# Performance work log

Measured on AMD Instinct MI355X. Metric: run time of the kernel, lower is better.

## Reference

```python
import jax, jax.numpy as jnp
import numpy as np

B_, J_, D_, E_, N_, K_ = 32, 1024, 192, 384, 16, 3


def _dwconv(x, w, b):
    # x: (B,J,E), w: (E,1,K) depthwise, b: (E,)
    xc = jnp.transpose(x, (0, 2, 1))  # (B,E,J)
    pad = w.shape[2] // 2
    y = jax.lax.conv_general_dilated(
        xc, w, window_strides=(1,), padding=[(pad, pad)],
        feature_group_count=w.shape[0], dimension_numbers=('NCH', 'OIH', 'NCH'))
    return jnp.transpose(y + b[None, :, None], (0, 2, 1))  # (B,J,E)


def _scan_dir(x, cw, cb, WB, bB, WC, bC, WD, bD, A, Wi, bi, Wr, br):
    # One directional selective-SSM pass. x: (B,J,E); A: (N,) negative diag.
    xc = _dwconv(x, cw, cb)                       # (B,J,E)
    Bt = xc @ WB + bB                             # (B,J,N)
    Ct = xc @ WC + bC                             # (B,J,N)
    Dt = jax.nn.softplus(xc @ WD + bD)            # Delta, (B,J,N)
    A_bar = jnp.exp(Dt * A)                       # ZOH discretization
    B_bar = (A_bar - 1.0) / (A + 1e-6) * Bt
    u = xc @ Wi + bi                              # in_to_state, (B,J,N)
    Bu = B_bar * u

    def step(h, ab_bu):
        ab, bu = ab_bu
        h = ab * h + bu
        return h, h

    h0 = jnp.zeros((x.shape[0], A.shape[0]), x.dtype)
    _, hs = jax.lax.scan(step, h0, (jnp.swapaxes(A_bar, 0, 1), jnp.swapaxes(Bu, 0, 1)))
    hs = jnp.swapaxes(hs, 0, 1)                   # (B,J,N)
    return (hs * Ct) @ Wr + br                    # readout, (B,J,E)


def setup_inputs() -> dict:
    key = jax.random.key(0)
    ks = iter(jax.random.split(key, 40))

    def nrm(shape, scale=0.02):
        return jax.random.normal(next(ks), shape, jnp.float32) * scale

    inp = {
        'tokens': jax.random.normal(next(ks), (B_, J_, D_), jnp.float32),
        'norm_g': jnp.ones((D_,), jnp.float32),
        'norm_b': jnp.zeros((D_,), jnp.float32),
        'Wx': nrm((D_, E_)), 'bx': jnp.zeros((E_,), jnp.float32),
        'Wz': nrm((D_, E_)), 'bz': jnp.zeros((E_,), jnp.float32),
        'convf_w': nrm((E_, 1, K_), 0.1), 'convf_b': jnp.zeros((E_,), jnp.float32),
        'convb_w': nrm((E_, 1, K_), 0.1), 'convb_b': jnp.zeros((E_,), jnp.float32),
        'WBf': nrm((E_, N_)), 'bBf': jnp.zeros((N_,), jnp.float32),
        'WCf': nrm((E_, N_)), 'bCf': jnp.zeros((N_,), jnp.float32),
        'WDf': nrm((E_, N_)), 'bDf': jnp.zeros((N_,), jnp.float32),
        'WBb': nrm((E_, N_)), 'bBb': jnp.zeros((N_,), jnp.float32),
        'WCb': nrm((E_, N_)), 'bCb': jnp.zeros((N_,), jnp.float32),
        'WDb': nrm((E_, N_)), 'bDb': jnp.zeros((N_,), jnp.float32),
        'A_log': nrm((N_,), 0.5),
        'Wi': nrm((E_, N_)), 'bi': jnp.zeros((N_,), jnp.float32),
        'Wr': nrm((N_, E_)), 'br': jnp.zeros((E_,), jnp.float32),
        'Wo': nrm((E_, D_)), 'bo': jnp.zeros((D_,), jnp.float32),
    }
    return inp


def reference(tokens, norm_g, norm_b, Wx, bx, Wz, bz, convf_w, convf_b,
              convb_w, convb_b, WBf, bBf, WCf, bCf, WDf, bDf, WBb, bBb,
              WCb, bCb, WDb, bDb, A_log, Wi, bi, Wr, br, Wo, bo):
    # LayerNorm (biased variance, eps=1e-5, like torch)
    mu = jnp.mean(tokens, axis=-1, keepdims=True)
    var = jnp.mean(jnp.square(tokens - mu), axis=-1, keepdims=True)
    t = (tokens - mu) / jnp.sqrt(var + 1e-5) * norm_g + norm_b

    x = t @ Wx + bx
    z = t @ Wz + bz
    gate = jax.nn.sigmoid(jax.nn.silu(z))

    # A computed under no_grad in torch -> stop_gradient here
    A = jax.lax.stop_gradient(-jax.nn.softplus(A_log))

    y_f = _scan_dir(x, convf_w, convf_b, WBf, bBf, WCf, bCf, WDf, bDf, A, Wi, bi, Wr, br)
    y_b = jnp.flip(_scan_dir(jnp.flip(x, 1), convb_w, convb_b, WBb, bBb, WCb, bCb,
                             WDb, bDb, A, Wi, bi, Wr, br), 1)
    y = (y_f + y_b) * gate
    return tokens + y @ Wo + bo
```

## Files before the change

kernel.cpp:

```cpp
#include <hip/hip_runtime.h>
#include <math.h>


typedef __attribute__((ext_vector_type(8))) short short8;
typedef __attribute__((ext_vector_type(4))) float f32x4;

__device__ __forceinline__ unsigned short f2bf(float f){
  union { float f; unsigned u; } v; v.f = f;
  unsigned r = v.u + 0x7FFFu + ((v.u >> 16) & 1u);
  return (unsigned short)(r >> 16);
}
__device__ __forceinline__ float bf2f(unsigned short s){
  union { unsigned u; float f; } v; v.u = ((unsigned)s) << 16;
  return v.f;
}
__device__ __forceinline__ float softplusf(float x){
  return (x > 20.f) ? x : log1pf(expf(x));
}
__device__ __forceinline__ float sigf_fast(float x){
  return __builtin_amdgcn_rcpf(1.f + __expf(-x));
}

__global__ __launch_bounds__(256) void prep_kernel(
    const float* __restrict__ Wx, const float* __restrict__ Wz,
    const float* __restrict__ WBf, const float* __restrict__ WCf,
    const float* __restrict__ WDf, const float* __restrict__ WBb,
    const float* __restrict__ WCb, const float* __restrict__ WDb,
    const float* __restrict__ Wi, const float* __restrict__ Wr,
    const float* __restrict__ Wo,
    const float* __restrict__ bBf, const float* __restrict__ bCf,
    const float* __restrict__ bDf, const float* __restrict__ bBb,
    const float* __restrict__ bCb, const float* __restrict__ bDb,
    const float* __restrict__ bi,
    unsigned short* __restrict__ Wxz_t, unsigned short* __restrict__ W4f_t,
    unsigned short* __restrict__ W4b_t, unsigned short* __restrict__ Wrt2,
    unsigned short* __restrict__ Wot, float* __restrict__ b4f,
    float* __restrict__ b4b)
{
  int idx = blockIdx.x * 256 + threadIdx.x;
  if (idx < 147456){ int n = idx / 192, k = idx % 192;
    Wxz_t[idx] = f2bf(n < 384 ? Wx[k*384 + n] : Wz[k*384 + n - 384]); return; }
  idx -= 147456;
  if (idx < 24576){ int n = idx / 384, k = idx % 384;
    const float* W = (n<16)?WBf:(n<32)?WCf:(n<48)?WDf:Wi;
    W4f_t[idx] = f2bf(W[k*16 + (n&15)]); return; }
  idx -= 24576;
  if (idx < 24576){ int n = idx / 384, k = idx % 384;
    const float* W = (n<16)?WBb:(n<32)?WCb:(n<48)?WDb:Wi;
    W4b_t[idx] = f2bf(W[k*16 + (n&15)]); return; }
  idx -= 24576;
  if (idx < 12288){ int n = idx / 32, k = idx % 32;
    Wrt2[idx] = f2bf(Wr[(k&15)*384 + n]); return; }
  idx -= 12288;
  if (idx < 73728){ int n = idx / 384, k = idx % 384;
    Wot[idx] = f2bf(Wo[k*192 + n]); return; }
  idx -= 73728;
  if (idx < 64){
    const float* bsel = (idx<16)?bBf:(idx<32)?bCf:(idx<48)?bDf:bi;
    b4f[idx] = bsel[idx & 15]; return; }
  idx -= 64;
  if (idx < 64){
    const float* bsel = (idx<16)?bBb:(idx<32)?bCb:(idx<48)?bDb:bi;
    b4b[idx] = bsel[idx & 15]; return; }
}

__global__ __launch_bounds__(256, 2) void ln_xz_mfma(
    const float* __restrict__ tokens, const float* __restrict__ g,
    const float* __restrict__ nb, const unsigned short* __restrict__ Wxz_t,
    const float* __restrict__ bx, const float* __restrict__ bz,
    unsigned short* __restrict__ x_bf, unsigned short* __restrict__ gate_bf)
{
  __shared__ unsigned short t_lds[64 * 200];
  const int t = threadIdx.x;
  const int ch = blockIdx.x & 1;
  const int row0 = (blockIdx.x >> 1) * 64;

  {
#pragma unroll
    for (int p = 0; p < 2; p++){
      const int r = p*32 + (t >> 3), l8 = t & 7;
      const float* tr = tokens + (long)(row0 + r) * 192;
      float v[24], s = 0.f, sq = 0.f;
#pragma unroll
      for (int i = 0; i < 24; i++){ float x = tr[l8 + 8*i]; v[i] = x; s += x; sq += x*x; }
#pragma unroll
      for (int m = 1; m < 8; m <<= 1){ s += __shfl_xor(s, m); sq += __shfl_xor(sq, m); }
      const float mu = s * (1.f/192.f);
      const float rstd = rsqrtf(sq * (1.f/192.f) - mu*mu + 1e-5f);
#pragma unroll
      for (int i = 0; i < 24; i++){
        const int d = l8 + 8*i;
        t_lds[r*200 + d] = f2bf((v[i] - mu)*rstd*g[d] + nb[d]);
      }
    }
  }
  __syncthreads();

  const int lane = t & 63, w = t >> 6;
  const int c0 = w * 96;
  const int l15 = lane & 15, q = lane >> 4;
  f32x4 acc[4][6];
#pragma unroll
  for (int m = 0; m < 4; m++)
#pragma unroll
    for (int n = 0; n < 6; n++) acc[m][n] = (f32x4){0.f,0.f,0.f,0.f};

  const unsigned short* wb = Wxz_t + (long)(ch*384 + c0 + l15)*192 + q*8;
#pragma unroll
  for (int ks = 0; ks < 6; ks++){
    const int k0 = ks * 32;
    short8 a0 = *(const short8*)&t_lds[(     l15)*200 + k0 + q*8];
    short8 a1 = *(const short8*)&t_lds[(16 + l15)*200 + k0 + q*8];
    short8 a2 = *(const short8*)&t_lds[(32 + l15)*200 + k0 + q*8];
    short8 a3 = *(const short8*)&t_lds[(48 + l15)*200 + k0 + q*8];
#pragma unroll
    for (int nf = 0; nf < 6; nf++){
      short8 bw = *(const short8*)&wb[nf*16*192 + k0];
      acc[0][nf] = __builtin_amdgcn_mfma_f32_16x16x32_bf16(a0, bw, acc[0][nf], 0, 0, 0);
      acc[1][nf] = __builtin_amdgcn_mfma_f32_16x16x32_bf16(a1, bw, acc[1][nf], 0, 0, 0);
      acc[2][nf] = __builtin_amdgcn_mfma_f32_16x16x32_bf16(a2, bw, acc[2][nf], 0, 0, 0);
      acc[3][nf] = __builtin_amdgcn_mfma_f32_16x16x32_bf16(a3, bw, acc[3][nf], 0, 0, 0);
    }
  }
  __syncthreads();

  const float* bias = ch ? bz : bx;
  unsigned short* outp = ch ? gate_bf : x_bf;
  unsigned short* stage = t_lds;

#pragma unroll
  for (int pp = 0; pp < 2; pp++){
#pragma unroll
    for (int mm = 0; mm < 2; mm++){
      const int m = pp*2 + mm;
#pragma unroll
      for (int nf = 0; nf < 6; nf++){
        const int lc = c0 + nf*16 + l15;
        const int scol = c0 + ((nf + q) % 6)*16 + l15;
        const float bv = bias[lc];
        if (ch == 0){
#pragma unroll
          for (int r = 0; r < 4; r++)
            stage[(mm*16 + q*4 + r)*392 + scol] = f2bf(acc[m][nf][r] + bv);
        } else {
#pragma unroll
          for (int r = 0; r < 4; r++){
            const float z = acc[m][nf][r] + bv;
            const float si = z * sigf_fast(z);
            stage[(mm*16 + q*4 + r)*392 + scol] = f2bf(sigf_fast(si));
          }
        }
      }
    }
    __syncthreads();
    {
#pragma unroll
      for (int i = 0; i < 6; i++){
        const int item = i*256 + t;
        const int row  = item / 48;
        const int c_out = (item % 48) * 8;
        const int qq = (row >> 2) & 3;
        const int wsl = c_out / 96;
        const int nfl = (c_out % 96) / 16;
        const int scol = wsl*96 + ((nfl + qq) % 6)*16 + (c_out % 16);
        short8 v = *(const short8*)&stage[row*392 + scol];
        const long R = (long)row0 + pp*32 + row;
        *(short8*)&outp[R*384 + c_out] = v;
      }
    }
    __syncthreads();
  }
}

__global__ __launch_bounds__(256) void proj_mfma(
    const unsigned short* __restrict__ x_bf,
    const float* __restrict__ cwf, const float* __restrict__ cbf,
    const float* __restrict__ cwb, const float* __restrict__ cbb,
    const unsigned short* __restrict__ W4f, const unsigned short* __restrict__ W4b,
    const float* __restrict__ b4f, const float* __restrict__ b4b,
    const float* __restrict__ A_log,
    float* __restrict__ Af, float* __restrict__ Buf, float* __restrict__ Ctf,
    float* __restrict__ Ab, float* __restrict__ Bub, float* __restrict__ Ctb)
{
  __shared__ unsigned short xc[64 * 392];
  float* trans = (float*)xc;
  const int t = threadIdx.x;
  const int dir = blockIdx.x >> 9;
  const int bid = blockIdx.x & 511;
  const int b  = bid >> 4;
  const int j0 = (bid & 15) * 64;
  const float* cw = dir ? cwb : cwf;
  const float* cb = dir ? cbb : cbf;
  const unsigned short* W4 = dir ? W4b : W4f;
  const float* b4 = dir ? b4b : b4f;
  float* Aout = dir ? Ab  : Af;
  float* Bout = dir ? Bub : Buf;
  float* Cout = dir ? Ctb : Ctf;

  {
    const long xrow = (long)b * 1024 * 384;
#pragma unroll
    for (int i = 0; i < 12; i++){
      const int idx = i*256 + t;
      const int r = idx / 48;
      const int e0 = (idx - r*48) * 8;
      const int jp = j0 + r;
      short8 xm = (short8){0,0,0,0,0,0,0,0};
      short8 xp = (short8){0,0,0,0,0,0,0,0};
      if (jp >= 1){
        const int js = dir ? 1024 - jp : jp - 1;
        xm = *(const short8*)&x_bf[xrow + (long)js*384 + e0];
      }
      short8 x0;
      {
        const int js = dir ? 1023 - jp : jp;
        x0 = *(const short8*)&x_bf[xrow + (long)js*384 + e0];
      }
      if (jp <= 1022){
        const int js = dir ? 1022 - jp : jp + 1;
        xp = *(const short8*)&x_bf[xrow + (long)js*384 + e0];
      }
      float wv[24], cbv[8];
#pragma unroll
      for (int v = 0; v < 6; v++)
        *(float4*)&wv[v*4] = *(const float4*)&cw[e0*3 + v*4];
#pragma unroll
      for (int v = 0; v < 2; v++)
        *(float4*)&cbv[v*4] = *(const float4*)&cb[e0 + v*4];
      short8 o;
#pragma unroll
      for (int m = 0; m < 8; m++){
        const float acc = fmaf(wv[3*m],   bf2f((unsigned short)xm[m]),
                          fmaf(wv[3*m+1], bf2f((unsigned short)x0[m]),
                          fmaf(wv[3*m+2], bf2f((unsigned short)xp[m]), cbv[m])));
        o[m] = (short)f2bf(acc);
      }
      *(short8*)&xc[r*392 + e0] = o;
    }
  }
  __syncthreads();

  const int lane = t & 63, w = t >> 6;
  const int l15 = lane & 15, q = lane >> 4;
  f32x4 acc[4];
#pragma unroll
  for (int nf = 0; nf < 4; nf++) acc[nf] = (f32x4){0.f,0.f,0.f,0.f};
  const unsigned short* wb = W4 + (long)l15*384 + q*8;
#pragma unroll
  for (int ks = 0; ks < 12; ks++){
    const int k0 = ks * 32;
    short8 a = *(const short8*)&xc[(w*16 + l15)*392 + k0 + q*8];
#pragma unroll
    for (int nf = 0; nf < 4; nf++){
      short8 bw = *(const short8*)&wb[nf*16*384 + k0];
      acc[nf] = __builtin_amdgcn_mfma_f32_16x16x32_bf16(a, bw, acc[nf], 0, 0, 0);
    }
  }
  __syncthreads();

  {
    const int n = l15;
    const float Av = -softplusf(A_log[n]);
    const float bB = b4[n], bC = b4[16+n], bD = b4[32+n], bU = b4[48+n];
#pragma unroll
    for (int r = 0; r < 4; r++){
      const int row = w*16 + q*4 + r;
      const float Bt  = acc[0][r] + bB;
      const float Ctv = acc[1][r] + bC;
      const float dt  = softplusf(acc[2][r] + bD);
      const float u   = acc[3][r] + bU;
      const float ab  = expf(dt * Av);
      const float bu  = (ab - 1.f) / (Av + 1e-6f) * Bt * u;
      trans[(0*16 + n)*66 + row] = ab;
      trans[(1*16 + n)*66 + row] = bu;
      trans[(2*16 + n)*66 + row] = Ctv;
    }
  }
  __syncthreads();

  {
    const int j = t & 63, n4 = t >> 6;
#pragma unroll
    for (int i = 0; i < 4; i++){
      const int n = n4*4 + i;
      const int jp = j0 + j;
      const long base = ((long)b*16 + n) * 1024;
      Aout[base + jp] = trans[(0*16 + n)*66 + j];
      Bout[base + jp] = trans[(1*16 + n)*66 + j];
      Cout[base + (dir ? 1023 - jp : jp)] = trans[(2*16 + n)*66 + j];
    }
  }
}

__global__ __launch_bounds__(256) void scan2_kernel(
    const float* __restrict__ Af, const float* __restrict__ Buf, float* __restrict__ hsf,
    const float* __restrict__ Ab, const float* __restrict__ Bub, float* __restrict__ hsb)
{
  __shared__ float sA[256], sB[256];
  const int sel = blockIdx.x >> 9;
  const long base = (long)(blockIdx.x & 511) * 1024;
  const float* Abar = sel ? Ab  : Af;
  const float* Bu   = sel ? Bub : Buf;
  float* hs         = sel ? hsb : hsf;
  const int t = threadIdx.x;
  const float4 a4 = *reinterpret_cast<const float4*>(&Abar[base + t*4]);
  const float4 b4 = *reinterpret_cast<const float4*>(&Bu[base + t*4]);
  float A = a4.x, Bc = b4.x;
  Bc = fmaf(a4.y, Bc, b4.y); A *= a4.y;
  Bc = fmaf(a4.z, Bc, b4.z); A *= a4.z;
  Bc = fmaf(a4.w, Bc, b4.w); A *= a4.w;
  sA[t] = A; sB[t] = Bc;
  __syncthreads();
  for (int off = 1; off < 256; off <<= 1){
    const float cA = sA[t], cB = sB[t];
    float pA = 1.f, pB = 0.f;
    if (t >= off){ pA = sA[t - off]; pB = sB[t - off]; }
    __syncthreads();
    sA[t] = pA * cA;
    sB[t] = fmaf(cA, pB, cB);
    __syncthreads();
  }
  float h = (t > 0) ? sB[t - 1] : 0.f;
  float4 o;
  h = fmaf(a4.x, h, b4.x); o.x = h;
  h = fmaf(a4.y, h, b4.y); o.y = h;
  h = fmaf(a4.z, h, b4.z); o.z = h;
  h = fmaf(a4.w, h, b4.w); o.w = h;
  *reinterpret_cast<float4*>(&hs[base + t*4]) = o;
}

__global__ __launch_bounds__(256) void final_mfma(
    const float* __restrict__ tokens, const unsigned short* __restrict__ gate_bf,
    const float* __restrict__ hsf, const float* __restrict__ Ctf,
    const float* __restrict__ hsb, const float* __restrict__ Ctb,
    const unsigned short* __restrict__ Wrt2, const float* __restrict__ br,
    const unsigned short* __restrict__ Wot, const float* __restrict__ bo,
    float* __restrict__ out)
{
  __shared__ unsigned short s2[32 * 40];
  __shared__ unsigned short yg[32 * 392];
  const int t = threadIdx.x;
  const int b  = blockIdx.x >> 5;
  const int j0 = (blockIdx.x & 31) * 32;

  {
#pragma unroll
    for (int i = 0; i < 4; i++){
      const int idx = i*256 + t;
      const int j = idx & 31, kk = idx >> 5;
      float val;
      if (kk < 16){
        const long p = ((long)b*16 + kk)*1024 + j0 + j;
        val = hsf[p] * Ctf[p];
      } else {
        const long basen = ((long)b*16 + (kk - 16)) * 1024;
        val = hsb[basen + 1023 - (j0 + j)] * Ctb[basen + j0 + j];
      }
      s2[j*40 + kk] = f2bf(val);
    }
  }
  __syncthreads();

  const int lane = t & 63, w = t >> 6;
  const int l15 = lane & 15, q = lane >> 4;
  const int rt = w & 1;
  const int ng = w >> 1;

  {
    short8 a = *(const short8*)&s2[(rt*16 + l15)*40 + q*8];
    const unsigned short* wbp = Wrt2 + (long)l15*32 + q*8;
#pragma unroll
    for (int i = 0; i < 12; i++){
      const int nf = ng*12 + i;
      short8 bw = *(const short8*)&wbp[nf*16*32];
      f32x4 acc = (f32x4){0.f,0.f,0.f,0.f};
      acc = __builtin_amdgcn_mfma_f32_16x16x32_bf16(a, bw, acc, 0, 0, 0);
      const int c = nf*16 + l15;
      const float brv = 2.f * br[c];
#pragma unroll
      for (int r = 0; r < 4; r++)
        yg[(rt*16 + q*4 + r)*392 + c] = f2bf(acc[r] + brv);
    }
  }
  __syncthreads();

  {
#pragma unroll
    for (int i = 0; i < 6; i++){
      const int item = i*256 + t;
      const int row = item / 48;
      const int cb  = (item % 48) * 8;
      short8 y8 = *(const short8*)&yg[row*392 + cb];
      short8 g8 = *(const short8*)&gate_bf[((long)b*1024 + j0 + row)*384 + cb];
      short8 o;
#pragma unroll
      for (int m = 0; m < 8; m++)
        o[m] = (short)f2bf(bf2f((unsigned short)y8[m]) * bf2f((unsigned short)g8[m]));
      *(short8*)&yg[row*392 + cb] = o;
    }
  }
  __syncthreads();

  f32x4 acc[6];
  {
#pragma unroll
    for (int i = 0; i < 6; i++) acc[i] = (f32x4){0.f,0.f,0.f,0.f};
    const unsigned short* wbp = Wot + (long)l15*384 + q*8;
#pragma unroll
    for (int ks = 0; ks < 12; ks++){
      const int k0 = ks * 32;
      short8 a = *(const short8*)&yg[(rt*16 + l15)*392 + k0 + q*8];
#pragma unroll
      for (int i = 0; i < 6; i++){
        const int nf = ng*6 + i;
        short8 bw = *(const short8*)&wbp[(long)nf*16*384 + k0];
        acc[i] = __builtin_amdgcn_mfma_f32_16x16x32_bf16(a, bw, acc[i], 0, 0, 0);
      }
    }
  }
  __syncthreads();

  float* stg = (float*)yg;
  {
    const int gq = q ^ (q >> 1);
#pragma unroll
    for (int i = 0; i < 6; i++){
      const int nf = ng*6 + i;
      const int c = nf*16 + l15;
      const float bv = bo[c];
      const int scol = ((nf + gq) % 12)*16 + l15;
#pragma unroll
      for (int r = 0; r < 4; r++)
        stg[(rt*16 + q*4 + r)*196 + scol] = acc[i][r] + bv;
    }
  }
  __syncthreads();

  {
#pragma unroll
    for (int i = 0; i < 6; i++){
      const int item = i*256 + t;
      const int row = item / 48;
      const int c4  = (item % 48) * 4;
      const int qq = (row >> 2) & 3;
      const int gg = qq ^ (qq >> 1);
      const int nf = c4 / 16;
      const int scol = ((nf + gg) % 12)*16 + (c4 % 16);
      float4 v = *(const float4*)&stg[row*196 + scol];
      const long R = (long)b*1024 + j0 + row;
      const float4 tk = *(const float4*)&tokens[R*192 + c4];
      v.x += tk.x; v.y += tk.y; v.z += tk.z; v.w += tk.w;
      *(float4*)&out[R*192 + c4] = v;
    }
  }
}

extern "C" void kernel_launch(void* const* d_in, const int* in_sizes, int n_in,
                              void* d_out, int out_size, void* d_ws, size_t ws_size,
                              hipStream_t stream)
{
  const float* tokens  = (const float*)d_in[0];
  const float* norm_g  = (const float*)d_in[1];
  const float* norm_b  = (const float*)d_in[2];
  const float* Wx      = (const float*)d_in[3];
  const float* bx      = (const float*)d_in[4];
  const float* Wz      = (const float*)d_in[5];
  const float* bz      = (const float*)d_in[6];
  const float* convf_w = (const float*)d_in[7];
  const float* convf_b = (const float*)d_in[8];
  const float* convb_w = (const float*)d_in[9];
  const float* convb_b = (const float*)d_in[10];
  const float* WBf     = (const float*)d_in[11];
  const float* bBf     = (const float*)d_in[12];
  const float* WCf     = (const float*)d_in[13];
  const float* bCf     = (const float*)d_in[14];
  const float* WDf     = (const float*)d_in[15];
  const float* bDf     = (const float*)d_in[16];
  const float* WBb     = (const float*)d_in[17];
  const float* bBb     = (const float*)d_in[18];
  const float* WCb     = (const float*)d_in[19];
  const float* bCb     = (const float*)d_in[20];
  const float* WDb     = (const float*)d_in[21];
  const float* bDb     = (const float*)d_in[22];
  const float* A_log   = (const float*)d_in[23];
  const float* Wi      = (const float*)d_in[24];
  const float* bi      = (const float*)d_in[25];
  const float* Wr      = (const float*)d_in[26];
  const float* br      = (const float*)d_in[27];
  const float* Wo      = (const float*)d_in[28];
  const float* bo      = (const float*)d_in[29];

  char* ws = (char*)d_ws;
  unsigned short* x_bf    = (unsigned short*)(ws + 0);
  unsigned short* gate_bf = (unsigned short*)(ws + 25165824);
  unsigned short* Wxz_t   = (unsigned short*)(ws + 50331648);
  unsigned short* W4f_t   = (unsigned short*)(ws + 50626560);
  unsigned short* W4b_t   = (unsigned short*)(ws + 50675712);
  unsigned short* Wrt2    = (unsigned short*)(ws + 50724864);
  unsigned short* Wot     = (unsigned short*)(ws + 50749440);
  float* b4f = (float*)(ws + 50896896);
  float* b4b = (float*)(ws + 50897152);
  float* Af  = (float*)(ws + 50897408);
  float* Buf = (float*)(ws + 52994560);
  float* Ctf = (float*)(ws + 55091712);
  float* hsf = (float*)(ws + 57188864);
  float* Ab  = (float*)(ws + 59286016);
  float* Bub = (float*)(ws + 61383168);
  float* Ctb = (float*)(ws + 63480320);
  float* hsb = (float*)(ws + 65577472);

  prep_kernel<<<1105, 256, 0, stream>>>(Wx, Wz, WBf, WCf, WDf, WBb, WCb, WDb,
                                        Wi, Wr, Wo, bBf, bCf, bDf, bBb, bCb, bDb, bi,
                                        Wxz_t, W4f_t, W4b_t, Wrt2, Wot, b4f, b4b);
  ln_xz_mfma<<<1024, 256, 0, stream>>>(tokens, norm_g, norm_b, Wxz_t, bx, bz,
                                       x_bf, gate_bf);
  proj_mfma<<<1024, 256, 0, stream>>>(x_bf, convf_w, convf_b, convb_w, convb_b,
                                      W4f_t, W4b_t, b4f, b4b, A_log,
                                      Af, Buf, Ctf, Ab, Bub, Ctb);
  scan2_kernel<<<1024, 256, 0, stream>>>(Af, Buf, hsf, Ab, Bub, hsb);
  final_mfma<<<1024, 256, 0, stream>>>(tokens, gate_bf, hsf, Ctf, hsb, Ctb,
                                       Wrt2, br, Wot, bo, (float*)d_out);
}
```

Measured before the change: 147.1 us.

## Split LayerNorm from x/z GEMM and retile GEMM to 64x128 column tiles

```diff
diff --git a/kernel.cpp b/kernel.cpp
--- a/kernel.cpp
+++ b/kernel.cpp
@@ -64,57 +64,84 @@
     b4b[idx] = bsel[idx & 15]; return; }
 }
 
-__global__ __launch_bounds__(256, 2) void ln_xz_mfma(
+__global__ __launch_bounds__(256) void ln_kernel(
     const float* __restrict__ tokens, const float* __restrict__ g,
-    const float* __restrict__ nb, const unsigned short* __restrict__ Wxz_t,
+    const float* __restrict__ nb, unsigned short* __restrict__ t_bf)
+{
+  __shared__ unsigned short s[32 * 200];
+  const int t = threadIdx.x;
+  const int row0 = blockIdx.x * 32;
+  {
+    const int r = t >> 3, l8 = t & 7;
+    const float* tr = tokens + (long)(row0 + r) * 192;
+    float v[24], sm = 0.f, sq = 0.f;
+#pragma unroll
+    for (int i = 0; i < 24; i++){ float x = tr[l8 + 8*i]; v[i] = x; sm += x; sq += x*x; }
+#pragma unroll
+    for (int m = 1; m < 8; m <<= 1){ sm += __shfl_xor(sm, m); sq += __shfl_xor(sq, m); }
+    const float mu = sm * (1.f/192.f);
+    const float rstd = rsqrtf(sq * (1.f/192.f) - mu*mu + 1e-5f);
+#pragma unroll
+    for (int i = 0; i < 24; i++){
+      const int d = l8 + 8*i;
+      s[r*200 + d] = f2bf((v[i] - mu)*rstd*g[d] + nb[d]);
+    }
+  }
+  __syncthreads();
+  {
+#pragma unroll
+    for (int i = 0; i < 3; i++){
+      const int item = i*256 + t;
+      const int row = item / 24, c8 = item % 24;
+      *(short8*)&t_bf[(long)(row0 + row)*192 + c8*8] =
+          *(const short8*)&s[row*200 + c8*8];
+    }
+  }
+}
+
+__global__ __launch_bounds__(256) void xz_gemm(
+    const unsigned short* __restrict__ t_bf,
+    const unsigned short* __restrict__ Wxz_t,
     const float* __restrict__ bx, const float* __restrict__ bz,
     unsigned short* __restrict__ x_bf, unsigned short* __restrict__ gate_bf)
 {
-  __shared__ unsigned short t_lds[64 * 200];
+  __shared__ unsigned short tl[64 * 200];
   const int t = threadIdx.x;
-  const int ch = blockIdx.x & 1;
-  const int row0 = (blockIdx.x >> 1) * 64;
-
-  {
-#pragma unroll
-    for (int p = 0; p < 2; p++){
-      const int r = p*32 + (t >> 3), l8 = t & 7;
-      const float* tr = tokens + (long)(row0 + r) * 192;
-      float v[24], s = 0.f, sq = 0.f;
-#pragma unroll
-      for (int i = 0; i < 24; i++){ float x = tr[l8 + 8*i]; v[i] = x; s += x; sq += x*x; }
-#pragma unroll
-      for (int m = 1; m < 8; m <<= 1){ s += __shfl_xor(s, m); sq += __shfl_xor(sq, m); }
-      const float mu = s * (1.f/192.f);
-      const float rstd = rsqrtf(sq * (1.f/192.f) - mu*mu + 1e-5f);
-#pragma unroll
-      for (int i = 0; i < 24; i++){
-        const int d = l8 + 8*i;
-        t_lds[r*200 + d] = f2bf((v[i] - mu)*rstd*g[d] + nb[d]);
-      }
+  const int ct = blockIdx.x % 6;
+  const int rt = blockIdx.x / 6;
+  const int row0 = rt * 64;
+
+  {
+#pragma unroll
+    for (int i = 0; i < 6; i++){
+      const int item = i*256 + t;
+      const int row = item / 24, c8 = item % 24;
+      *(short8*)&tl[row*200 + c8*8] =
+          *(const short8*)&t_bf[(long)(row0 + row)*192 + c8*8];
     }
   }
   __syncthreads();
 
   const int lane = t & 63, w = t >> 6;
-  const int c0 = w * 96;
   const int l15 = lane & 15, q = lane >> 4;
-  f32x4 acc[4][6];
+  const int C0 = ct*128 + w*32;
+
+  f32x4 acc[4][2];
 #pragma unroll
   for (int m = 0; m < 4; m++)
 #pragma unroll
-    for (int n = 0; n < 6; n++) acc[m][n] = (f32x4){0.f,0.f,0.f,0.f};
-
-  const unsigned short* wb = Wxz_t + (long)(ch*384 + c0 + l15)*192 + q*8;
+    for (int nf = 0; nf < 2; nf++) acc[m][nf] = (f32x4){0.f,0.f,0.f,0.f};
+
+  const unsigned short* wb = Wxz_t + (long)(C0 + l15)*192 + q*8;
 #pragma unroll
   for (int ks = 0; ks < 6; ks++){
     const int k0 = ks * 32;
-    short8 a0 = *(const short8*)&t_lds[(     l15)*200 + k0 + q*8];
-    short8 a1 = *(const short8*)&t_lds[(16 + l15)*200 + k0 + q*8];
-    short8 a2 = *(const short8*)&t_lds[(32 + l15)*200 + k0 + q*8];
-    short8 a3 = *(const short8*)&t_lds[(48 + l15)*200 + k0 + q*8];
-#pragma unroll
-    for (int nf = 0; nf < 6; nf++){
+    short8 a0 = *(const short8*)&tl[(     l15)*200 + k0 + q*8];
+    short8 a1 = *(const short8*)&tl[(16 + l15)*200 + k0 + q*8];
+    short8 a2 = *(const short8*)&tl[(32 + l15)*200 + k0 + q*8];
+    short8 a3 = *(const short8*)&tl[(48 + l15)*200 + k0 + q*8];
+#pragma unroll
+    for (int nf = 0; nf < 2; nf++){
       short8 bw = *(const short8*)&wb[nf*16*192 + k0];
       acc[0][nf] = __builtin_amdgcn_mfma_f32_16x16x32_bf16(a0, bw, acc[0][nf], 0, 0, 0);
       acc[1][nf] = __builtin_amdgcn_mfma_f32_16x16x32_bf16(a1, bw, acc[1][nf], 0, 0, 0);
@@ -124,51 +151,34 @@
   }
   __syncthreads();
 
-  const float* bias = ch ? bz : bx;
-  unsigned short* outp = ch ? gate_bf : x_bf;
-  unsigned short* stage = t_lds;
-
-#pragma unroll
-  for (int pp = 0; pp < 2; pp++){
-#pragma unroll
-    for (int mm = 0; mm < 2; mm++){
-      const int m = pp*2 + mm;
-#pragma unroll
-      for (int nf = 0; nf < 6; nf++){
-        const int lc = c0 + nf*16 + l15;
-        const int scol = c0 + ((nf + q) % 6)*16 + l15;
-        const float bv = bias[lc];
-        if (ch == 0){
-#pragma unroll
-          for (int r = 0; r < 4; r++)
-            stage[(mm*16 + q*4 + r)*392 + scol] = f2bf(acc[m][nf][r] + bv);
-        } else {
-#pragma unroll
-          for (int r = 0; r < 4; r++){
-            const float z = acc[m][nf][r] + bv;
-            const float si = z * sigf_fast(z);
-            stage[(mm*16 + q*4 + r)*392 + scol] = f2bf(sigf_fast(si));
-          }
-        }
-      }
-    }
-    __syncthreads();
-    {
-#pragma unroll
-      for (int i = 0; i < 6; i++){
-        const int item = i*256 + t;
-        const int row  = item / 48;
-        const int c_out = (item % 48) * 8;
-        const int qq = (row >> 2) & 3;
-        const int wsl = c_out / 96;
-        const int nfl = (c_out % 96) / 16;
-        const int scol = wsl*96 + ((nfl + qq) % 6)*16 + (c_out % 16);
-        short8 v = *(const short8*)&stage[row*392 + scol];
-        const long R = (long)row0 + pp*32 + row;
-        *(short8*)&outp[R*384 + c_out] = v;
-      }
-    }
-    __syncthreads();
+  unsigned short* stg = tl;
+  const int isgate = (ct >= 3);
+#pragma unroll
+  for (int nf = 0; nf < 2; nf++){
+    const int c = C0 + nf*16 + l15;
+    const float bv = isgate ? bz[c - 384] : bx[c];
+#pragma unroll
+    for (int m = 0; m < 4; m++){
+#pragma unroll
+      for (int r = 0; r < 4; r++){
+        float val = acc[m][nf][r] + bv;
+        if (isgate){ const float si = val * sigf_fast(val); val = sigf_fast(si); }
+        stg[(m*16 + q*4 + r)*136 + (w*32 + nf*16 + l15)] = f2bf(val);
+      }
+    }
+  }
+  __syncthreads();
+
+  {
+    unsigned short* outp = isgate ? gate_bf : x_bf;
+    const int cb = isgate ? (ct*128 - 384) : (ct*128);
+#pragma unroll
+    for (int i = 0; i < 4; i++){
+      const int item = i*256 + t;
+      const int row = item / 16, c8 = item % 16;
+      *(short8*)&outp[(long)(row0 + row)*384 + cb + c8*8] =
+          *(const short8*)&stg[row*136 + c8*8];
+    }
   }
 }
 
@@ -508,12 +518,13 @@
   float* Bub = (float*)(ws + 61383168);
   float* Ctb = (float*)(ws + 63480320);
   float* hsb = (float*)(ws + 65577472);
+  unsigned short* t_bf = (unsigned short*)(ws + 67674624);
 
   prep_kernel<<<1105, 256, 0, stream>>>(Wx, Wz, WBf, WCf, WDf, WBb, WCb, WDb,
                                         Wi, Wr, Wo, bBf, bCf, bDf, bBb, bCb, bDb, bi,
                                         Wxz_t, W4f_t, W4b_t, Wrt2, Wot, b4f, b4b);
-  ln_xz_mfma<<<1024, 256, 0, stream>>>(tokens, norm_g, norm_b, Wxz_t, bx, bz,
-                                       x_bf, gate_bf);
+  ln_kernel<<<1024, 256, 0, stream>>>(tokens, norm_g, norm_b, t_bf);
+  xz_gemm<<<3072, 256, 0, stream>>>(t_bf, Wxz_t, bx, bz, x_bf, gate_bf);
   proj_mfma<<<1024, 256, 0, stream>>>(x_bf, convf_w, convf_b, convb_w, convb_b,
                                       W4f_t, W4b_t, b4f, b4b, A_log,
                                       Af, Buf, Ctf, Ab, Bub, Ctb);
```

Result: faster. 141.5 us (-3.8%).
